# Kernel optimization log

Measured on AMD Instinct MI355X. Metric: run time of the kernel, lower is better.

Reference implementation:

```python
import jax, jax.numpy as jnp
import numpy as np

EPS = 1e-12  # F.normalize eps


def _lstm_dir(x, Wih_d, Whh_d, b_d, reverse):
    # x: [M, dim]; Wih_d/Whh_d: [4*dim, dim]; b_d: [4*dim]
    dim = Whh_d.shape[1]
    def step(carry, xt):
        h, c = carry
        z = xt @ Wih_d.T + h @ Whh_d.T + b_d  # [4*dim]
        i, f, g, o = jnp.split(z, 4)
        i = jax.nn.sigmoid(i); f = jax.nn.sigmoid(f)
        g = jnp.tanh(g); o = jax.nn.sigmoid(o)
        c = f * c + i * g
        h = o * jnp.tanh(c)
        return (h, c), h
    init = (jnp.zeros((dim,), x.dtype), jnp.zeros((dim,), x.dtype))
    _, hs = jax.lax.scan(step, init, x, reverse=reverse)
    return hs  # [M, dim]


def _forward(fingerprints, adjacency, words, emb_fp, emb_word,
             Wg, bg, Wih, Whh, bih, bhh, Wc, bc, Wp, bp, Wo, bo, Wi, bi):
    # ---- GAT over compound graph ----
    xs = emb_fp[fingerprints]  # [N, dim]
    L_gat = Wg.shape[0]
    for i in range(L_gat):
        hs = jax.nn.relu(xs @ Wg[i].T + bg[i])          # [N, dim]
        w = hs @ hs.T                                    # [N, N]
        attn = w * adjacency
        denom = jnp.maximum(jnp.sum(jnp.abs(attn), axis=1, keepdims=True), EPS)
        xs = xs + (attn / denom) @ hs
    x = xs  # compound atom vectors [N, dim]

    # ---- bidirectional LSTM over protein words ----
    wv = emb_word[words]  # [M, dim]
    h_f = _lstm_dir(wv, Wih[0], Whh[0], bih[0] + bhh[0], reverse=False)
    h_b = _lstm_dir(wv, Wih[1], Whh[1], bih[1] + bhh[1], reverse=True)
    xs_rnn = jax.nn.relu(jnp.concatenate([h_f, h_b], axis=1))  # [M, 2*dim]

    # ---- cross attention pooling ----
    h = jax.nn.relu(x @ Wc.T + bc)         # [N, dim]
    hp = jax.nn.relu(xs_rnn @ Wp.T + bp)   # [M, dim]
    weights = h @ hp.T                     # [N, M]
    w_comp = jnp.mean(weights, axis=1)     # [N]  (mean over M)
    w_prot = jnp.mean(weights, axis=0)     # [M]
    y = w_comp[:, None] * h                # [N, dim]
    ys = w_prot[:, None] * hp              # [M, dim]
    compound_vector = jnp.mean(y, axis=0)[None, :]   # [1, dim]
    protein_vector = jnp.mean(ys, axis=0)[None, :]   # [1, dim]

    # ---- output MLP ----
    cat = jnp.concatenate([compound_vector, protein_vector], axis=1)  # [1, 2*dim]
    L_out = Wo.shape[0]
    for j in range(L_out):
        cat = jax.nn.relu(cat @ Wo[j].T + bo[j])
    interaction = cat @ Wi.T + bi  # [1, 2]
    return interaction, weights


def setup_inputs() -> dict:
    key = jax.random.key(0)
    ks = jax.random.split(key, 16)
    N, M, DIM = 4096, 4096, 128
    N_FP, N_WORD = 100000, 10000
    L_GAT, L_OUT = 3, 2
    s = 0.05
    return {
        "fingerprints": jax.random.randint(ks[0], (N,), 0, N_FP),
        "adjacency": jax.random.uniform(ks[1], (N, N), jnp.float32),
        "words": jax.random.randint(ks[2], (M,), 0, N_WORD),
        "emb_fp": jax.random.normal(ks[3], (N_FP, DIM), jnp.float32) * s,
        "emb_word": jax.random.normal(ks[4], (N_WORD, DIM), jnp.float32) * s,
        "Wg": jax.random.normal(ks[5], (L_GAT, DIM, DIM), jnp.float32) * s,
        "bg": jnp.zeros((L_GAT, DIM), jnp.float32),
        "Wih": jax.random.normal(ks[6], (2, 4 * DIM, DIM), jnp.float32) * s,
        "Whh": jax.random.normal(ks[7], (2, 4 * DIM, DIM), jnp.float32) * s,
        "bih": jnp.zeros((2, 4 * DIM), jnp.float32),
        "bhh": jnp.zeros((2, 4 * DIM), jnp.float32),
        "Wc": jax.random.normal(ks[8], (DIM, DIM), jnp.float32) * s,
        "bc": jnp.zeros((DIM,), jnp.float32),
        "Wp": jax.random.normal(ks[9], (DIM, 2 * DIM), jnp.float32) * s,
        "bp": jnp.zeros((DIM,), jnp.float32),
        "Wo": jax.random.normal(ks[10], (L_OUT, 2 * DIM, 2 * DIM), jnp.float32) * s,
        "bo": jnp.zeros((L_OUT, 2 * DIM), jnp.float32),
        "Wi": jax.random.normal(ks[11], (2, 2 * DIM), jnp.float32) * s,
        "bi": jnp.zeros((2,), jnp.float32),
    }


def reference(fingerprints, adjacency, words, emb_fp, emb_word,
              Wg, bg, Wih, Whh, bih, bhh, Wc, bc, Wp, bp, Wo, bo, Wi, bi):
    return _forward(fingerprints, adjacency, words, emb_fp, emb_word,
                    Wg, bg, Wih, Whh, bih, bhh, Wc, bc, Wp, bp, Wo, bo, Wi, bi)
```

## Files before the change

### kernel.cpp

```cpp
#include <hip/hip_runtime.h>
#include <hip/hip_bf16.h>
#include <math.h>

#define DIM 128

typedef float v2f __attribute__((ext_vector_type(2)));
typedef _Float16 v2h __attribute__((ext_vector_type(2)));
typedef _Float16 h8v __attribute__((ext_vector_type(8)));
typedef short s8v __attribute__((ext_vector_type(8)));
typedef float f4v __attribute__((ext_vector_type(4)));

template<int CTRL>
__device__ inline float dpp_movf(float v) {
  int x = __builtin_amdgcn_update_dpp(0, __float_as_int(v), CTRL, 0xF, 0xF, true);
  return __int_as_float(x);
}
template<int CTRL>
__device__ inline float dpp_xadd(float v) { return v + dpp_movf<CTRL>(v); }

__device__ inline float dot8u(uint4 a, uint4 b, float acc) {
#if __has_builtin(__builtin_amdgcn_fdot2)
  acc = __builtin_amdgcn_fdot2(__builtin_bit_cast(v2h, a.x), __builtin_bit_cast(v2h, b.x), acc, false);
  acc = __builtin_amdgcn_fdot2(__builtin_bit_cast(v2h, a.y), __builtin_bit_cast(v2h, b.y), acc, false);
  acc = __builtin_amdgcn_fdot2(__builtin_bit_cast(v2h, a.z), __builtin_bit_cast(v2h, b.z), acc, false);
  acc = __builtin_amdgcn_fdot2(__builtin_bit_cast(v2h, a.w), __builtin_bit_cast(v2h, b.w), acc, false);
#else
  const v2h* pa = (const v2h*)&a; const v2h* pb = (const v2h*)&b;
#pragma unroll
  for (int i = 0; i < 4; ++i) {
    acc += (float)pa[i][0] * (float)pb[i][0];
    acc += (float)pa[i][1] * (float)pb[i][1];
  }
#endif
  return acc;
}

__device__ inline unsigned pk2h(float a, float b) {
  return __builtin_bit_cast(unsigned, __builtin_amdgcn_cvt_pkrtz(a, b));
}
__device__ inline float sigm_fast(float z) {
  return __builtin_amdgcn_rcpf(1.f + __expf(-z));
}
__device__ inline float tanh_fast(float z) {
  float e = __expf(-2.f * z);
  return (1.f - e) * __builtin_amdgcn_rcpf(1.f + e);
}
__device__ inline ushort f2bf(float x) {
  unsigned u = __builtin_bit_cast(unsigned, x);
  return (ushort)((u + 0x7FFFu + ((u >> 16) & 1u)) >> 16);
}

__global__ void gather_rows(const float* __restrict__ table, const int* __restrict__ idx,
                            float* __restrict__ dst, int n) {
  int i = blockIdx.x * blockDim.x + threadIdx.x;
  int total = n * 32;
  if (i >= total) return;
  int r = i >> 5, c = i & 31;
  const float4* src = (const float4*)table + (size_t)idx[r] * 32 + c;
  ((float4*)dst)[i] = *src;
}

__global__ void conv_f16(const float* __restrict__ src, _Float16* __restrict__ dst, int n4) {
  int i = blockIdx.x * blockDim.x + threadIdx.x;
  if (i >= n4) return;
  float4 v = ((const float4*)src)[i];
  ((uint2*)dst)[i] = make_uint2(pk2h(v.x, v.y), pk2h(v.z, v.w));
}

template<bool RELU, bool HASBIAS, bool HASADJ, bool PERMB>
__global__ __launch_bounds__(256) void gemm_nt(
    const float* __restrict__ A, const float* __restrict__ B,
    float* __restrict__ C, int ldc, int K,
    const float* __restrict__ bias,
    const float* __restrict__ adj, int ldadj)
{
  __shared__ float As[64][17];
  __shared__ float Bs[64][17];
  int tid = threadIdx.x;
  int tx = tid & 15, ty = tid >> 4;
  int rowBase = blockIdx.y * 64, colBase = blockIdx.x * 64;
  int lr = tid >> 2, lk = (tid & 3) * 4;
  int brow = colBase + lr;
  if (PERMB) brow = 128 * (brow & 3) + (brow >> 2);
  float acc[4][4] = {};
  for (int k0 = 0; k0 < K; k0 += 16) {
    float4 av = *(const float4*)&A[(size_t)(rowBase + lr) * K + k0 + lk];
    float4 bv = *(const float4*)&B[(size_t)brow * K + k0 + lk];
    As[lr][lk+0]=av.x; As[lr][lk+1]=av.y; As[lr][lk+2]=av.z; As[lr][lk+3]=av.w;
    Bs[lr][lk+0]=bv.x; Bs[lr][lk+1]=bv.y; Bs[lr][lk+2]=bv.z; Bs[lr][lk+3]=bv.w;
    __syncthreads();
#pragma unroll
    for (int kk = 0; kk < 16; ++kk) {
      float a0=As[ty*4+0][kk], a1=As[ty*4+1][kk], a2=As[ty*4+2][kk], a3=As[ty*4+3][kk];
      float b0=Bs[tx*4+0][kk], b1=Bs[tx*4+1][kk], b2=Bs[tx*4+2][kk], b3=Bs[tx*4+3][kk];
      acc[0][0]+=a0*b0; acc[0][1]+=a0*b1; acc[0][2]+=a0*b2; acc[0][3]+=a0*b3;
      acc[1][0]+=a1*b0; acc[1][1]+=a1*b1; acc[1][2]+=a1*b2; acc[1][3]+=a1*b3;
      acc[2][0]+=a2*b0; acc[2][1]+=a2*b1; acc[2][2]+=a2*b2; acc[2][3]+=a2*b3;
      acc[3][0]+=a3*b0; acc[3][1]+=a3*b1; acc[3][2]+=a3*b2; acc[3][3]+=a3*b3;
    }
    __syncthreads();
  }
  int row = rowBase + ty*4, col = colBase + tx*4;
#pragma unroll
  for (int i = 0; i < 4; ++i) {
    float aj[4] = {1.f,1.f,1.f,1.f};
    if (HASADJ) {
      float4 adjv = *(const float4*)&adj[(size_t)(row+i)*ldadj + col];
      aj[0]=adjv.x; aj[1]=adjv.y; aj[2]=adjv.z; aj[3]=adjv.w;
    }
    float v[4];
#pragma unroll
    for (int j = 0; j < 4; ++j) {
      float x = acc[i][j];
      if (HASBIAS) {
        int bidx = col + j;
        if (PERMB) bidx = 128 * (bidx & 3) + (bidx >> 2);
        x += bias[bidx];
      }
      if (HASADJ) x *= aj[j];
      if (RELU) x = fmaxf(x, 0.f);
      v[j] = x;
    }
    float* cp = &C[(size_t)(row+i)*ldc + col];
    *(float2*)cp = make_float2(v[0], v[1]);
    *(float2*)(cp+2) = make_float2(v[2], v[3]);
  }
}

__global__ void conv_bf16_T(const float* __restrict__ src, ushort* __restrict__ d1,
                            ushort* __restrict__ dT, int n) {
  int i = blockIdx.x * blockDim.x + threadIdx.x;
  if (i >= n * DIM) return;
  int r = i >> 7, d = i & 127;
  ushort v = f2bf(src[i]);
  d1[i] = v;
  dT[(size_t)d * n + r] = v;
}

#define LDT 136
__global__ __launch_bounds__(256) void mfma_nt_adj(
    const ushort* __restrict__ A, const ushort* __restrict__ B,
    ushort* __restrict__ C, int ldc,
    const float* __restrict__ adj, int ldadj)
{
  __shared__ ushort As[128][LDT];
  __shared__ ushort Bs[128][LDT];
  int tid = threadIdx.x;
  int rowBase = blockIdx.y * 128, colBase = blockIdx.x * 128;
#pragma unroll
  for (int it = 0; it < 8; ++it) {
    int c = it * 256 + tid;
    int r = c >> 4, ch = (c & 15) * 8;
    *(uint4*)&As[r][ch] = *(const uint4*)&A[(size_t)(rowBase + r) * DIM + ch];
    *(uint4*)&Bs[r][ch] = *(const uint4*)&B[(size_t)(colBase + r) * DIM + ch];
  }
  __syncthreads();
  int lane = tid & 63;
  int wv = tid >> 6, wr = wv >> 1, wc = wv & 1;
  int lr = lane & 15, lk = (lane >> 4) * 8;
  f4v acc[4][4] = {};
#pragma unroll
  for (int kc = 0; kc < 4; ++kc) {
    s8v a[4], b[4];
#pragma unroll
    for (int i = 0; i < 4; ++i) {
      a[i] = *(const s8v*)&As[wr*64 + i*16 + lr][kc*32 + lk];
      b[i] = *(const s8v*)&Bs[wc*64 + i*16 + lr][kc*32 + lk];
    }
#pragma unroll
    for (int i = 0; i < 4; ++i)
#pragma unroll
      for (int j = 0; j < 4; ++j)
        acc[i][j] = __builtin_amdgcn_mfma_f32_16x16x32_bf16(a[i], b[j], acc[i][j], 0, 0, 0);
  }
  int rsub = (lane >> 4) * 4;
#pragma unroll
  for (int i = 0; i < 4; ++i)
#pragma unroll
    for (int j = 0; j < 4; ++j) {
      int col = colBase + wc*64 + j*16 + lr;
#pragma unroll
      for (int rg = 0; rg < 4; ++rg) {
        int row = rowBase + wr*64 + i*16 + rsub + rg;
        float v = acc[i][j][rg] * adj[(size_t)row * ldadj + col];
        C[(size_t)row * ldc + col] = f2bf(v);
      }
    }
}

__global__ __launch_bounds__(256) void mfma_nt_f32(
    const _Float16* __restrict__ A, const _Float16* __restrict__ B,
    float* __restrict__ C, int ldc)
{
  __shared__ ushort As[128][LDT];
  __shared__ ushort Bs[128][LDT];
  int tid = threadIdx.x;
  int rowBase = blockIdx.y * 128, colBase = blockIdx.x * 128;
#pragma unroll
  for (int it = 0; it < 8; ++it) {
    int c = it * 256 + tid;
    int r = c >> 4, ch = (c & 15) * 8;
    *(uint4*)&As[r][ch] = *(const uint4*)&A[(size_t)(rowBase + r) * DIM + ch];
    *(uint4*)&Bs[r][ch] = *(const uint4*)&B[(size_t)(colBase + r) * DIM + ch];
  }
  __syncthreads();
  int lane = tid & 63;
  int wv = tid >> 6, wr = wv >> 1, wc = wv & 1;
  int lr = lane & 15, lk = (lane >> 4) * 8;
  f4v acc[4][4] = {};
#pragma unroll
  for (int kc = 0; kc < 4; ++kc) {
    h8v a[4], b[4];
#pragma unroll
    for (int i = 0; i < 4; ++i) {
      a[i] = *(const h8v*)&As[wr*64 + i*16 + lr][kc*32 + lk];
      b[i] = *(const h8v*)&Bs[wc*64 + i*16 + lr][kc*32 + lk];
    }
#pragma unroll
    for (int i = 0; i < 4; ++i)
#pragma unroll
      for (int j = 0; j < 4; ++j)
        acc[i][j] = __builtin_amdgcn_mfma_f32_16x16x32_f16(a[i], b[j], acc[i][j], 0, 0, 0);
  }
  int rsub = (lane >> 4) * 4;
#pragma unroll
  for (int i = 0; i < 4; ++i)
#pragma unroll
    for (int j = 0; j < 4; ++j) {
      int col = colBase + wc*64 + j*16 + lr;
#pragma unroll
      for (int rg = 0; rg < 4; ++rg) {
        int row = rowBase + wr*64 + i*16 + rsub + rg;
        C[(size_t)row * ldc + col] = acc[i][j][rg];
      }
    }
}

__global__ __launch_bounds__(256) void mfma_wx(
    const _Float16* __restrict__ A,
    const _Float16* __restrict__ Bw,
    const float* __restrict__ bias,
    float* __restrict__ out)
{
  __shared__ ushort As[128][LDT];
  __shared__ ushort Bs[128][LDT];
  int tid = threadIdx.x;
  int m0 = blockIdx.y * 128, colBase = blockIdx.x * 128;
#pragma unroll
  for (int it = 0; it < 8; ++it) {
    int c = it * 256 + tid;
    int r = c >> 4, ch = (c & 15) * 8;
    *(uint4*)&As[r][ch] = *(const uint4*)&A[(size_t)(m0 + r) * DIM + ch];
    int j = colBase + r;
    int brow = 128 * (j & 3) + (j >> 2);
    *(uint4*)&Bs[r][ch] = *(const uint4*)&Bw[(size_t)brow * DIM + ch];
  }
  __syncthreads();
  int lane = tid & 63;
  int wv = tid >> 6, wr = wv >> 1, wc = wv & 1;
  int lr = lane & 15, lk = (lane >> 4) * 8;
  f4v acc[4][4] = {};
#pragma unroll
  for (int kc = 0; kc < 4; ++kc) {
    h8v a[4], b[4];
#pragma unroll
    for (int i = 0; i < 4; ++i) {
      a[i] = *(const h8v*)&As[wr*64 + i*16 + lr][kc*32 + lk];
      b[i] = *(const h8v*)&Bs[wc*64 + i*16 + lr][kc*32 + lk];
    }
#pragma unroll
    for (int i = 0; i < 4; ++i)
#pragma unroll
      for (int j = 0; j < 4; ++j)
        acc[i][j] = __builtin_amdgcn_mfma_f32_16x16x32_f16(a[i], b[j], acc[i][j], 0, 0, 0);
  }
  int rsub = (lane >> 4) * 4;
#pragma unroll
  for (int i = 0; i < 4; ++i)
#pragma unroll
    for (int j = 0; j < 4; ++j) {
      int col = colBase + wc*64 + j*16 + lr;
      int brow = 128 * (col & 3) + (col >> 2);
      float bv = bias[brow];
#pragma unroll
      for (int rg = 0; rg < 4; ++rg) {
        int row = m0 + wr*64 + i*16 + rsub + rg;
        out[(size_t)row * 512 + col] = acc[i][j][rg] + bv;
      }
    }
}

#define LDT2 72
__global__ __launch_bounds__(256) void mfma_av(
    const ushort* __restrict__ attnb, const ushort* __restrict__ hsT,
    float* __restrict__ pt, int chunk, int N)
{
  __shared__ ushort As[128][LDT2];
  __shared__ ushort Bs[128][LDT2];
  int tid = threadIdx.x;
  int n0 = blockIdx.x * 128;
  int m0 = blockIdx.y * chunk;
  int lane = tid & 63;
  int wv = tid >> 6, wr = wv >> 1, wc = wv & 1;
  int lr = lane & 15, lk = (lane >> 4) * 8;
  f4v acc[4][4] = {};
  for (int mt = 0; mt < chunk; mt += 64) {
#pragma unroll
    for (int it = 0; it < 4; ++it) {
      int c = it * 256 + tid;
      int r = c >> 3, ch = (c & 7) * 8;
      *(uint4*)&As[r][ch] = *(const uint4*)&attnb[(size_t)(n0 + r) * N + m0 + mt + ch];
      *(uint4*)&Bs[r][ch] = *(const uint4*)&hsT[(size_t)r * N + m0 + mt + ch];
    }
    __syncthreads();
#pragma unroll
    for (int kc = 0; kc < 2; ++kc) {
      s8v a[4], b[4];
#pragma unroll
      for (int i = 0; i < 4; ++i) {
        a[i] = *(const s8v*)&As[wr*64 + i*16 + lr][kc*32 + lk];
        b[i] = *(const s8v*)&Bs[wc*64 + i*16 + lr][kc*32 + lk];
      }
#pragma unroll
      for (int i = 0; i < 4; ++i)
#pragma unroll
        for (int j = 0; j < 4; ++j)
          acc[i][j] = __builtin_amdgcn_mfma_f32_16x16x32_bf16(a[i], b[j], acc[i][j], 0, 0, 0);
    }
    __syncthreads();
  }
  size_t base = ((size_t)blockIdx.y * N + n0) * DIM;
  int rsub = (lane >> 4) * 4;
#pragma unroll
  for (int i = 0; i < 4; ++i)
#pragma unroll
    for (int j = 0; j < 4; ++j) {
      int d = wc*64 + j*16 + lr;
#pragma unroll
      for (int rg = 0; rg < 4; ++rg) {
        int nn = wr*64 + i*16 + rsub + rg;
        pt[base + (size_t)nn * DIM + d] = acc[i][j][rg];
      }
    }
}

__global__ void row_reduce_abs_bf16(const ushort* __restrict__ W, int ld, int M,
                                    float* __restrict__ out, float eps) {
  int n = blockIdx.x;
  const ushort* row = W + (size_t)n * ld;
  float s = 0;
  for (int m = threadIdx.x * 8; m < M; m += 256 * 8) {
    uint4 v = *(const uint4*)&row[m];
    unsigned a[4] = {v.x, v.y, v.z, v.w};
#pragma unroll
    for (int q = 0; q < 4; ++q) {
      s += __int_as_float((int)((a[q] & 0x7FFFu) << 16));
      s += __int_as_float((int)(a[q] & 0x7FFF0000u));
    }
  }
  __shared__ float red[256];
  red[threadIdx.x] = s; __syncthreads();
  for (int k = 128; k > 0; k >>= 1) {
    if (threadIdx.x < k) red[threadIdx.x] += red[threadIdx.x + k];
    __syncthreads();
  }
  if (threadIdx.x == 0) out[n] = fmaxf(red[0], eps);
}

__global__ void row_mean(const float* __restrict__ W, int ld, int M,
                         float* __restrict__ out, float inv) {
  int n = blockIdx.x;
  const float* row = W + (size_t)n * ld;
  float s = 0;
  for (int m = threadIdx.x; m < M; m += 256) s += row[m];
  __shared__ float red[256];
  red[threadIdx.x] = s; __syncthreads();
  for (int k = 128; k > 0; k >>= 1) {
    if (threadIdx.x < k) red[threadIdx.x] += red[threadIdx.x + k];
    __syncthreads();
  }
  if (threadIdx.x == 0) out[n] = red[0] * inv;
}

__global__ void colmean_part(const float* __restrict__ W, int ld, int rows_per,
                             float* __restrict__ part, int M) {
  int m = blockIdx.x * blockDim.x + threadIdx.x;
  int n0 = blockIdx.y * rows_per;
  float s = 0;
  for (int n = 0; n < rows_per; ++n) s += W[(size_t)(n0 + n) * ld + m];
  part[(size_t)blockIdx.y * M + m] = s;
}
__global__ void colmean_fin(const float* __restrict__ part, int M, int nparts,
                            float* __restrict__ out, float inv) {
  int m = blockIdx.x * blockDim.x + threadIdx.x;
  float s = 0;
  for (int k = 0; k < nparts; ++k) s += part[(size_t)k * M + m];
  out[m] = s * inv;
}

__global__ void axpy_reduce(const float* __restrict__ pt, const float* __restrict__ denom,
                            float* __restrict__ xs, int total) {
  int i = blockIdx.x * blockDim.x + threadIdx.x;
  if (i >= total) return;
  float s = 0;
#pragma unroll
  for (int k = 0; k < 8; ++k) s += pt[(size_t)k * total + i];
  xs[i] += s / denom[i >> 7];
}

__global__ void add_vec(const float* __restrict__ a, const float* __restrict__ b,
                        float* __restrict__ o, int n) {
  int i = blockIdx.x * blockDim.x + threadIdx.x;
  if (i < n) o[i] = a[i] + b[i];
}

#define REP8(X) X(0) X(1) X(2) X(3) X(4) X(5) X(6) X(7)

__global__ __launch_bounds__(512, 2) void lstm_kernel(
    const float* __restrict__ Whh,
    const float* __restrict__ Wxp,
    float* __restrict__ xs_rnn,
    int M)
{
  int dir = blockIdx.x;
  int tid = threadIdx.x;
  int w = tid >> 6, lane = tid & 63;
  int u  = w * 16 + (lane >> 2);
  int gp = (lane >> 1) & 1;
  int kh = lane & 1;
  int row0 = gp ? (256 + u) : u;
  const float* base = Whh + (size_t)dir * 512 * DIM;
  const float4* w0p = (const float4*)(base + (size_t)row0 * DIM + kh * 64);
  const float4* w1p = (const float4*)(base + (size_t)(row0 + 128) * DIM + kh * 64);

#define DECLW(r) uint4 wA##r, wB##r;
  REP8(DECLW)
#define LOADW(r) { \
    float4 x = w0p[2*(r)], y = w0p[2*(r)+1]; \
    wA##r = make_uint4(pk2h(x.x,x.y), pk2h(x.z,x.w), pk2h(y.x,y.y), pk2h(y.z,y.w)); \
    x = w1p[2*(r)]; y = w1p[2*(r)+1]; \
    wB##r = make_uint4(pk2h(x.x,x.y), pk2h(x.z,x.w), pk2h(y.x,y.y), pk2h(y.z,y.w)); }
  REP8(LOADW)

  __shared__ __align__(16) _Float16 hbuf[2][DIM];
  if (tid < DIM) hbuf[0][tid] = (_Float16)0.f;
  float c = 0.f;
  __syncthreads();

  const float* WxD = Wxp + (size_t)dir * M * 512;
  int wxcol = 4 * u + 2 * gp;
  int t0 = dir ? (M - 1) : 0;
  float2 wx = *(const float2*)&WxD[(size_t)t0 * 512 + wxcol];
  for (int s = 0; s < M; ++s) {
    int t = dir ? (M - 1 - s) : s;
    float2 wxn = make_float2(0.f, 0.f);
    if (s + 1 < M) {
      int tn = dir ? (M - 2 - s) : (s + 1);
      wxn = *(const float2*)&WxD[(size_t)tn * 512 + wxcol];
    }
    int cur = s & 1;
    const uint4* hb = (const uint4*)(hbuf[cur]) + kh * 8;
    float a0 = 0.f, a1 = 0.f;
#define DOTW(r) { uint4 hv = hb[r]; a0 = dot8u(wA##r, hv, a0); a1 = dot8u(wB##r, hv, a1); }
    REP8(DOTW)
    float z0 = dpp_xadd<0xB1>(a0) + wx.x;
    float z1 = dpp_xadd<0xB1>(a1) + wx.y;
    float av0 = gp ? tanh_fast(z0) : sigm_fast(z0);
    float av1 = sigm_fast(z1);
    float gv = dpp_movf<0x102>(av0);
    float ov = dpp_movf<0x102>(av1);
    if ((lane & 3) == 0) {
      c = av1 * c + av0 * gv;
      float hv = ov * tanh_fast(c);
      hbuf[cur ^ 1][u] = (_Float16)hv;
      xs_rnn[(size_t)t * (2 * DIM) + dir * DIM + u] = fmaxf(hv, 0.f);
    }
    wx = wxn;
    __syncthreads();
  }
#undef DOTW
#undef LOADW
#undef DECLW
}

__global__ void pool_vec(const float* __restrict__ mat, const float* __restrict__ wv,
                         int n, float* __restrict__ out, float inv) {
  int t = threadIdx.x; int g = t >> 7, d = t & 127;
  float acc = 0;
  for (int r = g; r < n; r += 8) acc += wv[r] * mat[(size_t)r * DIM + d];
  __shared__ float red[1024];
  red[t] = acc; __syncthreads();
  if (g == 0) {
    float s = acc;
#pragma unroll
    for (int k = 1; k < 8; ++k) s += red[k * 128 + d];
    out[d] = s * inv;
  }
}

__global__ void mlp_kernel(const float* __restrict__ cvec, const float* __restrict__ pvec,
                           const float* __restrict__ Wo, const float* __restrict__ bo,
                           const float* __restrict__ Wi, const float* __restrict__ bi,
                           float* __restrict__ out) {
  __shared__ float buf0[256], buf1[256];
  int t = threadIdx.x;
  buf0[t] = (t < 128) ? cvec[t] : pvec[t - 128];
  __syncthreads();
  {
    const float* W = Wo;
    float s = bo[t];
    for (int v = 0; v < 256; ++v) s += W[t * 256 + v] * buf0[v];
    buf1[t] = fmaxf(s, 0.f);
  }
  __syncthreads();
  {
    const float* W = Wo + 256 * 256;
    float s = bo[256 + t];
    for (int v = 0; v < 256; ++v) s += W[t * 256 + v] * buf1[v];
    buf0[t] = fmaxf(s, 0.f);
  }
  __syncthreads();
  if (t < 2) {
    float s = bi[t];
    for (int v = 0; v < 256; ++v) s += Wi[t * 256 + v] * buf0[v];
    out[t] = s;
  }
}

extern "C" void kernel_launch(void* const* d_in, const int* in_sizes, int n_in,
                              void* d_out, int out_size, void* d_ws, size_t ws_size,
                              hipStream_t stream) {
  const int*   fingerprints = (const int*)d_in[0];
  const float* adjacency    = (const float*)d_in[1];
  const int*   words        = (const int*)d_in[2];
  const float* emb_fp       = (const float*)d_in[3];
  const float* emb_word     = (const float*)d_in[4];
  const float* Wg  = (const float*)d_in[5];
  const float* bg  = (const float*)d_in[6];
  const float* Wih = (const float*)d_in[7];
  const float* Whh = (const float*)d_in[8];
  const float* bih = (const float*)d_in[9];
  const float* bhh = (const float*)d_in[10];
  const float* Wc  = (const float*)d_in[11];
  const float* bc  = (const float*)d_in[12];
  const float* Wp  = (const float*)d_in[13];
  const float* bp  = (const float*)d_in[14];
  const float* Wo  = (const float*)d_in[15];
  const float* bo  = (const float*)d_in[16];
  const float* Wi  = (const float*)d_in[17];
  const float* bi  = (const float*)d_in[18];

  const int N = in_sizes[0];
  const int M = in_sizes[2];
  const int LGAT = in_sizes[5] / (DIM * DIM);

  float* out  = (float*)d_out;
  float* attn = out + 2;
  ushort* attnb = (ushort*)attn;

  float* ws = (float*)d_ws;
  size_t off = 0;
  auto alloc = [&](size_t nf) { float* p = ws + off; off += (nf + 3) & ~(size_t)3; return p; };
  float* xs     = alloc((size_t)N * DIM);
  float* hs     = alloc((size_t)N * DIM);
  float* wvb    = alloc((size_t)M * DIM);
  float* denom  = alloc(N);
  float* pt     = alloc((size_t)8 * N * DIM);
  float* Wx     = pt;
  float* xs_rnn = alloc((size_t)M * 2 * DIM);
  float* hp     = alloc((size_t)M * DIM);
  float* hmat   = alloc((size_t)N * DIM);
  float* bsum   = alloc(1024);
  float* wcomp  = alloc(N);
  float* wprot  = alloc(M);
  float* cvec   = alloc(DIM);
  float* pvec   = alloc(DIM);
  float* cpart  = alloc((size_t)32 * M);
  ushort* hs_b  = (ushort*)alloc((size_t)N * DIM / 2);
  ushort* hsT_b = (ushort*)alloc((size_t)N * DIM / 2);
  _Float16* wvb_h  = (_Float16*)alloc((size_t)M * DIM / 2);
  _Float16* wih_h  = (_Float16*)alloc((size_t)2 * 512 * DIM / 2);
  _Float16* hmat_h = (_Float16*)alloc((size_t)N * DIM / 2);
  _Float16* hp_h   = (_Float16*)alloc((size_t)M * DIM / 2);
  (void)ws_size; (void)n_in; (void)out_size;

  gather_rows<<<(N * 32 + 255) / 256, 256, 0, stream>>>(emb_fp, fingerprints, xs, N);
  gather_rows<<<(M * 32 + 255) / 256, 256, 0, stream>>>(emb_word, words, wvb, M);

  for (int l = 0; l < LGAT; ++l) {
    gemm_nt<true, true, false, false><<<dim3(DIM / 64, N / 64), 256, 0, stream>>>(
        xs, Wg + (size_t)l * DIM * DIM, hs, DIM, DIM, bg + l * DIM, nullptr, 0);
    conv_bf16_T<<<(N * DIM) / 256, 256, 0, stream>>>(hs, hs_b, hsT_b, N);
    mfma_nt_adj<<<dim3(N / 128, N / 128), 256, 0, stream>>>(
        hs_b, hs_b, attnb, N, adjacency, N);
    row_reduce_abs_bf16<<<N, 256, 0, stream>>>(attnb, N, N, denom, 1e-12f);
    mfma_av<<<dim3(N / 128, 8), 256, 0, stream>>>(attnb, hsT_b, pt, N / 8, N);
    axpy_reduce<<<(N * DIM) / 256, 256, 0, stream>>>(pt, denom, xs, N * DIM);
  }

  add_vec<<<4, 256, 0, stream>>>(bih, bhh, bsum, 1024);
  conv_f16<<<(M * DIM / 4 + 255) / 256, 256, 0, stream>>>(wvb, wvb_h, M * DIM / 4);
  conv_f16<<<(2 * 512 * DIM / 4 + 255) / 256, 256, 0, stream>>>(Wih, wih_h, 2 * 512 * DIM / 4);
  for (int d = 0; d < 2; ++d) {
    mfma_wx<<<dim3(512 / 128, M / 128), 256, 0, stream>>>(
        wvb_h, wih_h + (size_t)d * 512 * DIM, bsum + d * 512, Wx + (size_t)d * M * 512);
  }
  lstm_kernel<<<2, 512, 0, stream>>>(Whh, Wx, xs_rnn, M);

  gemm_nt<true, true, false, false><<<dim3(DIM / 64, M / 64), 256, 0, stream>>>(
      xs_rnn, Wp, hp, DIM, 2 * DIM, bp, nullptr, 0);
  gemm_nt<true, true, false, false><<<dim3(DIM / 64, N / 64), 256, 0, stream>>>(
      xs, Wc, hmat, DIM, DIM, bc, nullptr, 0);
  conv_f16<<<(N * DIM / 4 + 255) / 256, 256, 0, stream>>>(hmat, hmat_h, N * DIM / 4);
  conv_f16<<<(M * DIM / 4 + 255) / 256, 256, 0, stream>>>(hp, hp_h, M * DIM / 4);
  mfma_nt_f32<<<dim3(M / 128, N / 128), 256, 0, stream>>>(hmat_h, hp_h, attn, M);
  row_mean<<<N, 256, 0, stream>>>(attn, M, M, wcomp, 1.f / (float)M);
  colmean_part<<<dim3(M / 256, 32), 256, 0, stream>>>(attn, M, N / 32, cpart, M);
  colmean_fin<<<M / 256, 256, 0, stream>>>(cpart, M, 32, wprot, 1.f / (float)N);
  pool_vec<<<1, 1024, 0, stream>>>(hmat, wcomp, N, cvec, 1.f / (float)N);
  pool_vec<<<1, 1024, 0, stream>>>(hp, wprot, M, pvec, 1.f / (float)M);

  mlp_kernel<<<1, 256, 0, stream>>>(cvec, pvec, Wo, bo, Wi, bi, out);
}
```

Before: 2.924 ms.

## Fuse precision conversions into GEMM epilogues and gather, split LSTM dot accumulators

```diff
diff --git a/kernel.cpp b/kernel.cpp
--- a/kernel.cpp
+++ b/kernel.cpp
@@ -49,6 +49,9 @@
   unsigned u = __builtin_bit_cast(unsigned, x);
   return (ushort)((u + 0x7FFFu + ((u >> 16) & 1u)) >> 16);
 }
+__device__ inline unsigned pk2bf(float a, float b) {
+  return (unsigned)f2bf(a) | ((unsigned)f2bf(b) << 16);
+}
 
 __global__ void gather_rows(const float* __restrict__ table, const int* __restrict__ idx,
                             float* __restrict__ dst, int n) {
@@ -59,6 +62,16 @@
   const float4* src = (const float4*)table + (size_t)idx[r] * 32 + c;
   ((float4*)dst)[i] = *src;
 }
+__global__ void gather_rows_wv(const float* __restrict__ table, const int* __restrict__ idx,
+                               float* __restrict__ dst, _Float16* __restrict__ dsth, int n) {
+  int i = blockIdx.x * blockDim.x + threadIdx.x;
+  int total = n * 32;
+  if (i >= total) return;
+  int r = i >> 5, c = i & 31;
+  float4 v = ((const float4*)table)[(size_t)idx[r] * 32 + c];
+  ((float4*)dst)[i] = v;
+  ((uint2*)dsth)[i] = make_uint2(pk2h(v.x, v.y), pk2h(v.z, v.w));
+}
 
 __global__ void conv_f16(const float* __restrict__ src, _Float16* __restrict__ dst, int n4) {
   int i = blockIdx.x * blockDim.x + threadIdx.x;
@@ -67,12 +80,18 @@
   ((uint2*)dst)[i] = make_uint2(pk2h(v.x, v.y), pk2h(v.z, v.w));
 }
 
-template<bool RELU, bool HASBIAS, bool HASADJ, bool PERMB>
+__global__ void tr_bf16(const ushort* __restrict__ src, ushort* __restrict__ dT, int n) {
+  int i = blockIdx.x * blockDim.x + threadIdx.x;
+  if (i >= n * DIM) return;
+  int r = i >> 7, d = i & 127;
+  dT[(size_t)d * n + r] = src[i];
+}
+
+template<bool RELU, int OM>
 __global__ __launch_bounds__(256) void gemm_nt(
     const float* __restrict__ A, const float* __restrict__ B,
-    float* __restrict__ C, int ldc, int K,
-    const float* __restrict__ bias,
-    const float* __restrict__ adj, int ldadj)
+    float* __restrict__ C, ushort* __restrict__ Cb, _Float16* __restrict__ Ch,
+    int ldc, int K, const float* __restrict__ bias)
 {
   __shared__ float As[64][17];
   __shared__ float Bs[64][17];
@@ -80,12 +99,10 @@
   int tx = tid & 15, ty = tid >> 4;
   int rowBase = blockIdx.y * 64, colBase = blockIdx.x * 64;
   int lr = tid >> 2, lk = (tid & 3) * 4;
-  int brow = colBase + lr;
-  if (PERMB) brow = 128 * (brow & 3) + (brow >> 2);
   float acc[4][4] = {};
   for (int k0 = 0; k0 < K; k0 += 16) {
     float4 av = *(const float4*)&A[(size_t)(rowBase + lr) * K + k0 + lk];
-    float4 bv = *(const float4*)&B[(size_t)brow * K + k0 + lk];
+    float4 bv = *(const float4*)&B[(size_t)(colBase + lr) * K + k0 + lk];
     As[lr][lk+0]=av.x; As[lr][lk+1]=av.y; As[lr][lk+2]=av.z; As[lr][lk+3]=av.w;
     Bs[lr][lk+0]=bv.x; Bs[lr][lk+1]=bv.y; Bs[lr][lk+2]=bv.z; Bs[lr][lk+3]=bv.w;
     __syncthreads();
@@ -103,38 +120,24 @@
   int row = rowBase + ty*4, col = colBase + tx*4;
 #pragma unroll
   for (int i = 0; i < 4; ++i) {
-    float aj[4] = {1.f,1.f,1.f,1.f};
-    if (HASADJ) {
-      float4 adjv = *(const float4*)&adj[(size_t)(row+i)*ldadj + col];
-      aj[0]=adjv.x; aj[1]=adjv.y; aj[2]=adjv.z; aj[3]=adjv.w;
-    }
     float v[4];
 #pragma unroll
     for (int j = 0; j < 4; ++j) {
-      float x = acc[i][j];
-      if (HASBIAS) {
-        int bidx = col + j;
-        if (PERMB) bidx = 128 * (bidx & 3) + (bidx >> 2);
-        x += bias[bidx];
-      }
-      if (HASADJ) x *= aj[j];
+      float x = acc[i][j] + bias[col + j];
       if (RELU) x = fmaxf(x, 0.f);
       v[j] = x;
     }
-    float* cp = &C[(size_t)(row+i)*ldc + col];
-    *(float2*)cp = make_float2(v[0], v[1]);
-    *(float2*)(cp+2) = make_float2(v[2], v[3]);
-  }
-}
-
-__global__ void conv_bf16_T(const float* __restrict__ src, ushort* __restrict__ d1,
-                            ushort* __restrict__ dT, int n) {
-  int i = blockIdx.x * blockDim.x + threadIdx.x;
-  if (i >= n * DIM) return;
-  int r = i >> 7, d = i & 127;
-  ushort v = f2bf(src[i]);
-  d1[i] = v;
-  dT[(size_t)d * n + r] = v;
+    size_t base = (size_t)(row + i) * ldc + col;
+    if (OM == 1) {
+      *(uint2*)&Cb[base] = make_uint2(pk2bf(v[0], v[1]), pk2bf(v[2], v[3]));
+    } else {
+      float* cp = &C[base];
+      *(float2*)cp = make_float2(v[0], v[1]);
+      *(float2*)(cp+2) = make_float2(v[2], v[3]);
+      if (OM == 2)
+        *(uint2*)&Ch[base] = make_uint2(pk2h(v[0], v[1]), pk2h(v[2], v[3]));
+    }
+  }
 }
 
 #define LDT 136
@@ -413,8 +416,6 @@
   int i = blockIdx.x * blockDim.x + threadIdx.x;
   if (i < n) o[i] = a[i] + b[i];
 }
-
-#define REP8(X) X(0) X(1) X(2) X(3) X(4) X(5) X(6) X(7)
 
 __global__ __launch_bounds__(512, 2) void lstm_kernel(
     const float* __restrict__ Whh,
@@ -433,6 +434,7 @@
   const float4* w0p = (const float4*)(base + (size_t)row0 * DIM + kh * 64);
   const float4* w1p = (const float4*)(base + (size_t)(row0 + 128) * DIM + kh * 64);
 
+#define REP8(X) X(0) X(1) X(2) X(3) X(4) X(5) X(6) X(7)
 #define DECLW(r) uint4 wA##r, wB##r;
   REP8(DECLW)
 #define LOADW(r) { \
@@ -460,9 +462,22 @@
     }
     int cur = s & 1;
     const uint4* hb = (const uint4*)(hbuf[cur]) + kh * 8;
-    float a0 = 0.f, a1 = 0.f;
-#define DOTW(r) { uint4 hv = hb[r]; a0 = dot8u(wA##r, hv, a0); a1 = dot8u(wB##r, hv, a1); }
-    REP8(DOTW)
+    float a00 = 0.f, a01 = 0.f, a02 = 0.f, a03 = 0.f;
+    float a10 = 0.f, a11 = 0.f, a12 = 0.f, a13 = 0.f;
+    {
+      uint4 h0 = hb[0], h1 = hb[1], h2 = hb[2], h3 = hb[3];
+      uint4 h4 = hb[4], h5 = hb[5], h6 = hb[6], h7 = hb[7];
+      a00 = dot8u(wA0, h0, a00); a10 = dot8u(wB0, h0, a10);
+      a01 = dot8u(wA1, h1, a01); a11 = dot8u(wB1, h1, a11);
+      a02 = dot8u(wA2, h2, a02); a12 = dot8u(wB2, h2, a12);
+      a03 = dot8u(wA3, h3, a03); a13 = dot8u(wB3, h3, a13);
+      a00 = dot8u(wA4, h4, a00); a10 = dot8u(wB4, h4, a10);
+      a01 = dot8u(wA5, h5, a01); a11 = dot8u(wB5, h5, a11);
+      a02 = dot8u(wA6, h6, a02); a12 = dot8u(wB6, h6, a12);
+      a03 = dot8u(wA7, h7, a03); a13 = dot8u(wB7, h7, a13);
+    }
+    float a0 = (a00 + a01) + (a02 + a03);
+    float a1 = (a10 + a11) + (a12 + a13);
     float z0 = dpp_xadd<0xB1>(a0) + wx.x;
     float z1 = dpp_xadd<0xB1>(a1) + wx.y;
     float av0 = gp ? tanh_fast(z0) : sigm_fast(z0);
@@ -478,9 +493,9 @@
     wx = wxn;
     __syncthreads();
   }
-#undef DOTW
 #undef LOADW
 #undef DECLW
+#undef REP8
 }
 
 __global__ void pool_vec(const float* __restrict__ mat, const float* __restrict__ wv,
@@ -562,7 +577,6 @@
   size_t off = 0;
   auto alloc = [&](size_t nf) { float* p = ws + off; off += (nf + 3) & ~(size_t)3; return p; };
   float* xs     = alloc((size_t)N * DIM);
-  float* hs     = alloc((size_t)N * DIM);
   float* wvb    = alloc((size_t)M * DIM);
   float* denom  = alloc(N);
   float* pt     = alloc((size_t)8 * N * DIM);
@@ -585,12 +599,12 @@
   (void)ws_size; (void)n_in; (void)out_size;
 
   gather_rows<<<(N * 32 + 255) / 256, 256, 0, stream>>>(emb_fp, fingerprints, xs, N);
-  gather_rows<<<(M * 32 + 255) / 256, 256, 0, stream>>>(emb_word, words, wvb, M);
+  gather_rows_wv<<<(M * 32 + 255) / 256, 256, 0, stream>>>(emb_word, words, wvb, wvb_h, M);
 
   for (int l = 0; l < LGAT; ++l) {
-    gemm_nt<true, true, false, false><<<dim3(DIM / 64, N / 64), 256, 0, stream>>>(
-        xs, Wg + (size_t)l * DIM * DIM, hs, DIM, DIM, bg + l * DIM, nullptr, 0);
-    conv_bf16_T<<<(N * DIM) / 256, 256, 0, stream>>>(hs, hs_b, hsT_b, N);
+    gemm_nt<true, 1><<<dim3(DIM / 64, N / 64), 256, 0, stream>>>(
+        xs, Wg + (size_t)l * DIM * DIM, nullptr, hs_b, nullptr, DIM, DIM, bg + l * DIM);
+    tr_bf16<<<(N * DIM) / 256, 256, 0, stream>>>(hs_b, hsT_b, N);
     mfma_nt_adj<<<dim3(N / 128, N / 128), 256, 0, stream>>>(
         hs_b, hs_b, attnb, N, adjacency, N);
     row_reduce_abs_bf16<<<N, 256, 0, stream>>>(attnb, N, N, denom, 1e-12f);
@@ -599,7 +613,6 @@
   }
 
   add_vec<<<4, 256, 0, stream>>>(bih, bhh, bsum, 1024);
-  conv_f16<<<(M * DIM / 4 + 255) / 256, 256, 0, stream>>>(wvb, wvb_h, M * DIM / 4);
   conv_f16<<<(2 * 512 * DIM / 4 + 255) / 256, 256, 0, stream>>>(Wih, wih_h, 2 * 512 * DIM / 4);
   for (int d = 0; d < 2; ++d) {
     mfma_wx<<<dim3(512 / 128, M / 128), 256, 0, stream>>>(
@@ -607,12 +620,10 @@
   }
   lstm_kernel<<<2, 512, 0, stream>>>(Whh, Wx, xs_rnn, M);
 
-  gemm_nt<true, true, false, false><<<dim3(DIM / 64, M / 64), 256, 0, stream>>>(
-      xs_rnn, Wp, hp, DIM, 2 * DIM, bp, nullptr, 0);
-  gemm_nt<true, true, false, false><<<dim3(DIM / 64, N / 64), 256, 0, stream>>>(
-      xs, Wc, hmat, DIM, DIM, bc, nullptr, 0);
-  conv_f16<<<(N * DIM / 4 + 255) / 256, 256, 0, stream>>>(hmat, hmat_h, N * DIM / 4);
-  conv_f16<<<(M * DIM / 4 + 255) / 256, 256, 0, stream>>>(hp, hp_h, M * DIM / 4);
+  gemm_nt<true, 2><<<dim3(DIM / 64, M / 64), 256, 0, stream>>>(
+      xs_rnn, Wp, hp, nullptr, hp_h, DIM, 2 * DIM, bp);
+  gemm_nt<true, 2><<<dim3(DIM / 64, N / 64), 256, 0, stream>>>(
+      xs, Wc, hmat, nullptr, hmat_h, DIM, DIM, bc);
   mfma_nt_f32<<<dim3(M / 128, N / 128), 256, 0, stream>>>(hmat_h, hp_h, attn, M);
   row_mean<<<N, 256, 0, stream>>>(attn, M, M, wcomp, 1.f / (float)M);
   colmean_part<<<dim3(M / 256, 32), 256, 0, stream>>>(attn, M, N / 32, cpart, M);
```

Measured after the change: 3.178 ms. 8.7% more time.
